# Performance work log

Hardware: AMD Instinct MI355X
Metric: run time of the kernel (lower is better)

Reference implementation:

```python
import jax, jax.numpy as jnp
import numpy as np

N_NODES = 50000
N_EDGES = 600000
IN_DIM = 128
HID = 128
N_CLASSES = 40
N_GRAPHS = 128


def setup_inputs() -> dict:
    key = jax.random.key(0)
    ks = jax.random.split(key, 12)
    x = jax.random.normal(ks[0], (N_NODES, IN_DIM), dtype=jnp.float32)
    edge_index = jax.random.randint(ks[1], (2, N_EDGES), 0, N_NODES, dtype=jnp.int64)
    batch = jnp.sort(jax.random.randint(ks[2], (N_NODES,), 0, N_GRAPHS, dtype=jnp.int64))
    dims = [IN_DIM, HID, HID, N_CLASSES]
    params = {}
    for l in range(3):
        d_in, d_out = dims[l], dims[l + 1]
        s = 1.0 / np.sqrt(d_in)
        params[f"Wl{l}"] = jax.random.uniform(ks[3 + 3 * l], (d_out, d_in), jnp.float32, -s, s)
        params[f"bl{l}"] = jax.random.uniform(ks[4 + 3 * l], (d_out,), jnp.float32, -s, s)
        params[f"Wr{l}"] = jax.random.uniform(ks[5 + 3 * l], (d_out, d_in), jnp.float32, -s, s)
    return {"x": x, "edge_index": edge_index, "batch": batch, **params}


def _sage_layer(h, src, dst, Wl, bl, Wr):
    # message: relu(x_j) (edge_attr is None -> zero), mean-aggregate at dst
    m = jnp.maximum(h[src], 0.0)                       # [E, d]
    agg = jax.ops.segment_sum(m, dst, num_segments=N_NODES)
    cnt = jax.ops.segment_sum(jnp.ones((m.shape[0],), h.dtype), dst, num_segments=N_NODES)
    agg = agg / jnp.maximum(cnt, 1.0)[:, None]
    # lin_l(agg) + lin_r(x)
    return agg @ Wl.T + bl + h @ Wr.T


def reference(x, edge_index, batch, Wl0, bl0, Wr0, Wl1, bl1, Wr1, Wl2, bl2, Wr2):
    src, dst = edge_index[0], edge_index[1]
    Ws = [(Wl0, bl0, Wr0), (Wl1, bl1, Wr1), (Wl2, bl2, Wr2)]
    h = x
    for l, (Wl, bl, Wr) in enumerate(Ws):
        # dropout is identity in eval mode
        h = _sage_layer(h, src, dst, Wl, bl, Wr)
        if l != len(Ws) - 1:
            h = jnp.maximum(h, 0.0)
    # global mean pool over graphs
    gsum = jax.ops.segment_sum(h, batch, num_segments=N_GRAPHS)
    gcnt = jax.ops.segment_sum(jnp.ones((h.shape[0],), h.dtype), batch, num_segments=N_GRAPHS)
    g = gsum / jnp.maximum(gcnt, 1.0)[:, None]
    return h, g
```

## Files before the change

### kernel.cpp

```cpp
#include <hip/hip_runtime.h>
#include <hip/hip_bf16.h>


#define NODES 50000
#define K_DIM 128
#define N_GRAPHS 128

typedef __attribute__((ext_vector_type(8))) short short8;
typedef __attribute__((ext_vector_type(4))) short short4v;
typedef __attribute__((ext_vector_type(4))) float f32x4;

__device__ inline short f2bf(float f) {
    unsigned u = __builtin_bit_cast(unsigned, f);
    u += 0x7FFFu + ((u >> 16) & 1u);
    return (short)(u >> 16);
}
__device__ inline float bf2f(short h) {
    unsigned u = ((unsigned)(unsigned short)h) << 16;
    return __builtin_bit_cast(float, u);
}
__device__ inline float blo(unsigned u) { return __builtin_bit_cast(float, u << 16); }
__device__ inline float bhi(unsigned u) { return __builtin_bit_cast(float, u & 0xFFFF0000u); }
__device__ inline unsigned hilo_pack(float f) {
    short h = f2bf(f);
    short l = f2bf(f - bf2f(h));
    return ((unsigned)(unsigned short)h) | (((unsigned)(unsigned short)l) << 16);
}

__global__ void init_kernel(const float* __restrict__ w0, const float* __restrict__ w1,
                            const float* __restrict__ w2, const float* __restrict__ w3,
                            const float* __restrict__ w4, const float* __restrict__ w5,
                            short* __restrict__ whi, short* __restrict__ wlo,
                            int* __restrict__ deg, const int* __restrict__ batch,
                            int* __restrict__ gstart,
                            const float* __restrict__ x, short* __restrict__ xb, int N) {
    int idx = blockIdx.x * 256 + threadIdx.x;
    if (idx < N * (K_DIM / 4)) {
        float4 v = reinterpret_cast<const float4*>(x)[idx];
        short4v b;
        b[0] = f2bf(fmaxf(v.x, 0.f));
        b[1] = f2bf(fmaxf(v.y, 0.f));
        b[2] = f2bf(fmaxf(v.z, 0.f));
        b[3] = f2bf(fmaxf(v.w, 0.f));
        *reinterpret_cast<short4v*>(&xb[idx * 4]) = b;
    }
    if (idx < N) deg[idx] = 0;
    const int TOT = 4 * 16384 + 96 * 128;
    if (idx < TOT) {
        float v;
        if (idx < 65536) {
            int m = idx >> 14, e = idx & 16383;
            const float* W = (m == 0) ? w0 : (m == 1) ? w1 : (m == 2) ? w2 : w3;
            v = W[e];
        } else {
            int i2 = idx - 65536;
            int row = i2 >> 7, col = i2 & 127;
            if (row < 40)      v = w4[row * 128 + col];
            else if (row < 80) v = w5[(row - 40) * 128 + col];
            else               v = 0.f;
        }
        unsigned p = hilo_pack(v);
        whi[idx] = (short)(p & 0xFFFFu);
        wlo[idx] = (short)(p >> 16);
    }
    if (idx <= N_GRAPHS) {
        int g = idx;
        int lo = 0, hi = N;
        while (lo < hi) {
            int mid = (lo + hi) >> 1;
            if (batch[mid] < g) lo = mid + 1; else hi = mid;
        }
        gstart[g] = lo;
    }
}

__global__ void deg_kernel(const int* __restrict__ dst, int* __restrict__ deg, int E) {
    int e = blockIdx.x * blockDim.x + threadIdx.x;
    if (e < E) atomicAdd(&deg[dst[e]], 1);
}

__global__ void scan_p1(const int* __restrict__ deg, int* __restrict__ bsum, int N) {
    int i = blockIdx.x * 256 + threadIdx.x;
    int v = (i < N) ? deg[i] : 0;
    #pragma unroll
    for (int off = 32; off > 0; off >>= 1) v += __shfl_down(v, off, 64);
    __shared__ int ws[4];
    int lane = threadIdx.x & 63, wv = threadIdx.x >> 6;
    if (lane == 0) ws[wv] = v;
    __syncthreads();
    if (threadIdx.x == 0) bsum[blockIdx.x] = ws[0] + ws[1] + ws[2] + ws[3];
}

__global__ void scan_p23(const int* __restrict__ deg, const int* __restrict__ bsum,
                         int* __restrict__ rowptr, int* __restrict__ fillpos,
                         int N, int NB) {
    const int tid = threadIdx.x, lane = tid & 63, wv = tid >> 6;
    __shared__ int ws[4];
    __shared__ int sboff[256];
    {
        int v = (tid < NB) ? bsum[tid] : 0;
        int incl = v;
        #pragma unroll
        for (int off = 1; off < 64; off <<= 1) {
            int t = __shfl_up(incl, off, 64);
            if (lane >= off) incl += t;
        }
        if (lane == 63) ws[wv] = incl;
        __syncthreads();
        int add = 0;
        for (int k = 0; k < wv; ++k) add += ws[k];
        sboff[tid] = incl + add - v;
        __syncthreads();
    }
    const int boff = sboff[blockIdx.x];
    int i = blockIdx.x * 256 + tid;
    int v = (i < N) ? deg[i] : 0;
    int incl = v;
    #pragma unroll
    for (int off = 1; off < 64; off <<= 1) {
        int t = __shfl_up(incl, off, 64);
        if (lane >= off) incl += t;
    }
    __shared__ int ws2[4];
    if (lane == 63) ws2[wv] = incl;
    __syncthreads();
    int add = 0;
    for (int k = 0; k < wv; ++k) add += ws2[k];
    int excl = boff + incl + add - v;
    if (i < N) { rowptr[i] = excl; fillpos[i] = excl; }
    if (i == N) rowptr[N] = excl;
}

__global__ void fill_kernel(const int* __restrict__ src, const int* __restrict__ dst,
                            int* __restrict__ fillpos, int* __restrict__ csr_src, int E) {
    int e = blockIdx.x * blockDim.x + threadIdx.x;
    if (e < E) {
        int p = atomicAdd(&fillpos[dst[e]], 1);
        csr_src[p] = src[e];
    }
}

__global__ void agg_bf16(const unsigned short* __restrict__ hb,
                         const int* __restrict__ rowptr,
                         const int* __restrict__ csr_src,
                         float* __restrict__ agg, int N) {
    int w = (blockIdx.x * blockDim.x + threadIdx.x) >> 6;
    if (w >= N) return;
    int lane = threadIdx.x & 63;
    int half = lane >> 5, l32 = lane & 31;
    int s = rowptr[w], e = rowptr[w + 1];
    float4 acc = make_float4(0.f, 0.f, 0.f, 0.f);
    int i = s + half;
    for (; i + 6 < e; i += 8) {
        int s0 = csr_src[i], s1 = csr_src[i + 2], s2 = csr_src[i + 4], s3 = csr_src[i + 6];
        uint2 v0 = reinterpret_cast<const uint2*>(hb + (size_t)s0 * K_DIM)[l32];
        uint2 v1 = reinterpret_cast<const uint2*>(hb + (size_t)s1 * K_DIM)[l32];
        uint2 v2 = reinterpret_cast<const uint2*>(hb + (size_t)s2 * K_DIM)[l32];
        uint2 v3 = reinterpret_cast<const uint2*>(hb + (size_t)s3 * K_DIM)[l32];
        acc.x += (blo(v0.x) + blo(v1.x)) + (blo(v2.x) + blo(v3.x));
        acc.y += (bhi(v0.x) + bhi(v1.x)) + (bhi(v2.x) + bhi(v3.x));
        acc.z += (blo(v0.y) + blo(v1.y)) + (blo(v2.y) + blo(v3.y));
        acc.w += (bhi(v0.y) + bhi(v1.y)) + (bhi(v2.y) + bhi(v3.y));
    }
    for (; i < e; i += 2) {
        int s0 = csr_src[i];
        uint2 v0 = reinterpret_cast<const uint2*>(hb + (size_t)s0 * K_DIM)[l32];
        acc.x += blo(v0.x); acc.y += bhi(v0.x);
        acc.z += blo(v0.y); acc.w += bhi(v0.y);
    }
    acc.x += __shfl_xor(acc.x, 32, 64);
    acc.y += __shfl_xor(acc.y, 32, 64);
    acc.z += __shfl_xor(acc.z, 32, 64);
    acc.w += __shfl_xor(acc.w, 32, 64);
    if (half == 0) {
        float inv = 1.0f / fmaxf((float)(e - s), 1.0f);
        acc.x *= inv; acc.y *= inv; acc.z *= inv; acc.w *= inv;
        reinterpret_cast<float4*>(agg + (size_t)w * K_DIM)[l32] = acc;
    }
}

template <int WAVES_M, int WAVES_N, int WM_TILES, int WN_TILES, bool BF16OUT>
__global__ __launch_bounds__(256) void sage_mfma(
        const float* __restrict__ A, const float* __restrict__ H,
        const short* __restrict__ Bhl, const short* __restrict__ Bll,
        const short* __restrict__ Bhr, const short* __restrict__ Blr,
        const float* __restrict__ bl, float* __restrict__ out,
        short* __restrict__ outb, int N) {
    constexpr int BM = WAVES_M * WM_TILES * 16;
    constexpr int LSTR = 40;
    const int tid = threadIdx.x;
    const int lane = tid & 63;
    const int wave = tid >> 6;
    const int wm = wave % WAVES_M;
    const int wn = wave / WAVES_M;
    const int l15 = lane & 15;
    const int quad = lane >> 4;
    const int m0 = blockIdx.x * BM;

    __shared__ __align__(16) short Ahi[BM * LSTR];
    __shared__ __align__(16) short Alo[BM * LSTR];

    f32x4 acc[WM_TILES][WN_TILES];
    #pragma unroll
    for (int i = 0; i < WM_TILES; ++i)
        #pragma unroll
        for (int j = 0; j < WN_TILES; ++j)
            acc[i][j] = (f32x4){0.f, 0.f, 0.f, 0.f};

    #pragma unroll
    for (int ph = 0; ph < 2; ++ph) {
        const float* __restrict__ X = ph ? H : A;
        const short* __restrict__ Bh = ph ? Bhr : Bhl;
        const short* __restrict__ Bv = ph ? Blr : Bll;
        for (int k0 = 0; k0 < K_DIM; k0 += 32) {
            __syncthreads();
            #pragma unroll
            for (int r = 0; r < BM * 8 / 256; ++r) {
                int idx = r * 256 + tid;
                int row = idx >> 3, c4 = idx & 7;
                int m = m0 + row;
                float4 v = make_float4(0.f, 0.f, 0.f, 0.f);
                if (m < N) v = *reinterpret_cast<const float4*>(X + (size_t)m * K_DIM + k0 + c4 * 4);
                unsigned px = hilo_pack(v.x);
                unsigned py = hilo_pack(v.y);
                unsigned pz = hilo_pack(v.z);
                unsigned pw = hilo_pack(v.w);
                short4v h4, l4;
                h4[0] = (short)(px & 0xFFFFu); l4[0] = (short)(px >> 16);
                h4[1] = (short)(py & 0xFFFFu); l4[1] = (short)(py >> 16);
                h4[2] = (short)(pz & 0xFFFFu); l4[2] = (short)(pz >> 16);
                h4[3] = (short)(pw & 0xFFFFu); l4[3] = (short)(pw >> 16);
                *reinterpret_cast<short4v*>(&Ahi[row * LSTR + c4 * 4]) = h4;
                *reinterpret_cast<short4v*>(&Alo[row * LSTR + c4 * 4]) = l4;
            }
            short8 bh[WN_TILES], bo[WN_TILES];
            #pragma unroll
            for (int nt = 0; nt < WN_TILES; ++nt) {
                int n = wn * WN_TILES * 16 + nt * 16 + l15;
                bh[nt] = *reinterpret_cast<const short8*>(Bh + (size_t)n * K_DIM + k0 + quad * 8);
                bo[nt] = *reinterpret_cast<const short8*>(Bv + (size_t)n * K_DIM + k0 + quad * 8);
            }
            __syncthreads();
            #pragma unroll
            for (int mt = 0; mt < WM_TILES; ++mt) {
                int row = wm * WM_TILES * 16 + mt * 16 + l15;
                short8 ah = *reinterpret_cast<const short8*>(&Ahi[row * LSTR + quad * 8]);
                short8 ao = *reinterpret_cast<const short8*>(&Alo[row * LSTR + quad * 8]);
                #pragma unroll
                for (int nt = 0; nt < WN_TILES; ++nt) {
                    acc[mt][nt] = __builtin_amdgcn_mfma_f32_16x16x32_bf16(ah, bh[nt], acc[mt][nt], 0, 0, 0);
                    acc[mt][nt] = __builtin_amdgcn_mfma_f32_16x16x32_bf16(ah, bo[nt], acc[mt][nt], 0, 0, 0);
                    acc[mt][nt] = __builtin_amdgcn_mfma_f32_16x16x32_bf16(ao, bh[nt], acc[mt][nt], 0, 0, 0);
                }
            }
        }
    }

    #pragma unroll
    for (int mt = 0; mt < WM_TILES; ++mt) {
        #pragma unroll
        for (int nt = 0; nt < WN_TILES; ++nt) {
            int col = wn * WN_TILES * 16 + nt * 16 + l15;
            float b = bl[col];
            #pragma unroll
            for (int reg = 0; reg < 4; ++reg) {
                int row = m0 + wm * WM_TILES * 16 + mt * 16 + quad * 4 + reg;
                if (row < N) {
                    float v = fmaxf(acc[mt][nt][reg] + b, 0.f);
                    out[(size_t)row * K_DIM + col] = v;
                    if (BF16OUT) outb[(size_t)row * K_DIM + col] = f2bf(v);
                }
            }
        }
    }
}

__global__ __launch_bounds__(256) void gemm80(
        const float* __restrict__ X, const short* __restrict__ Bh,
        const short* __restrict__ Bv, const float* __restrict__ b2,
        short* __restrict__ ylb, float* __restrict__ yr40, int N) {
    constexpr int BM = 64;
    constexpr int LSTR = 40;
    const int tid = threadIdx.x;
    const int lane = tid & 63;
    const int wave = tid >> 6;
    const int wm = wave & 1;
    const int wn = wave >> 1;
    const int l15 = lane & 15;
    const int quad = lane >> 4;
    const int m0 = blockIdx.x * BM;

    __shared__ __align__(16) short Ahi[BM * LSTR];
    __shared__ __align__(16) short Alo[BM * LSTR];

    f32x4 acc[2][3];
    #pragma unroll
    for (int i = 0; i < 2; ++i)
        #pragma unroll
        for (int j = 0; j < 3; ++j) acc[i][j] = (f32x4){0.f, 0.f, 0.f, 0.f};

    for (int k0 = 0; k0 < K_DIM; k0 += 32) {
        __syncthreads();
        #pragma unroll
        for (int r = 0; r < 2; ++r) {
            int idx = r * 256 + tid;
            int row = idx >> 3, c4 = idx & 7;
            int m = m0 + row;
            float4 v = make_float4(0.f, 0.f, 0.f, 0.f);
            if (m < N) v = *reinterpret_cast<const float4*>(X + (size_t)m * K_DIM + k0 + c4 * 4);
            unsigned px = hilo_pack(v.x);
            unsigned py = hilo_pack(v.y);
            unsigned pz = hilo_pack(v.z);
            unsigned pw = hilo_pack(v.w);
            short4v h4, l4;
            h4[0] = (short)(px & 0xFFFFu); l4[0] = (short)(px >> 16);
            h4[1] = (short)(py & 0xFFFFu); l4[1] = (short)(py >> 16);
            h4[2] = (short)(pz & 0xFFFFu); l4[2] = (short)(pz >> 16);
            h4[3] = (short)(pw & 0xFFFFu); l4[3] = (short)(pw >> 16);
            *reinterpret_cast<short4v*>(&Ahi[row * LSTR + c4 * 4]) = h4;
            *reinterpret_cast<short4v*>(&Alo[row * LSTR + c4 * 4]) = l4;
        }
        __syncthreads();
        short8 bh[3], bo[3];
        #pragma unroll
        for (int nt = 0; nt < 3; ++nt) {
            int n = wn * 48 + nt * 16 + l15;
            bh[nt] = *reinterpret_cast<const short8*>(Bh + (size_t)n * K_DIM + k0 + quad * 8);
            bo[nt] = *reinterpret_cast<const short8*>(Bv + (size_t)n * K_DIM + k0 + quad * 8);
        }
        #pragma unroll
        for (int mt = 0; mt < 2; ++mt) {
            int row = wm * 32 + mt * 16 + l15;
            short8 ah = *reinterpret_cast<const short8*>(&Ahi[row * LSTR + quad * 8]);
            short8 ao = *reinterpret_cast<const short8*>(&Alo[row * LSTR + quad * 8]);
            #pragma unroll
            for (int nt = 0; nt < 3; ++nt) {
                acc[mt][nt] = __builtin_amdgcn_mfma_f32_16x16x32_bf16(ah, bh[nt], acc[mt][nt], 0, 0, 0);
                acc[mt][nt] = __builtin_amdgcn_mfma_f32_16x16x32_bf16(ah, bo[nt], acc[mt][nt], 0, 0, 0);
                acc[mt][nt] = __builtin_amdgcn_mfma_f32_16x16x32_bf16(ao, bh[nt], acc[mt][nt], 0, 0, 0);
            }
        }
    }

    #pragma unroll
    for (int mt = 0; mt < 2; ++mt) {
        #pragma unroll
        for (int nt = 0; nt < 3; ++nt) {
            int col = wn * 48 + nt * 16 + l15;
            #pragma unroll
            for (int reg = 0; reg < 4; ++reg) {
                int row = m0 + wm * 32 + mt * 16 + quad * 4 + reg;
                if (row < N) {
                    float v = acc[mt][nt][reg];
                    if (col < 40) {
                        ylb[(size_t)row * 40 + col] = f2bf(v);
                    } else if (col < 80) {
                        yr40[(size_t)row * 40 + (col - 40)] = v + b2[col - 40];
                    }
                }
            }
        }
    }
}

__global__ void agg40_kernel(const unsigned short* __restrict__ ylb,
                             const float* __restrict__ yr40,
                             const int* __restrict__ rowptr, const int* __restrict__ csr_src,
                             float* __restrict__ out, int N) {
    int w = (blockIdx.x * blockDim.x + threadIdx.x) >> 6;
    if (w >= N) return;
    int lane = threadIdx.x & 63;
    int s = rowptr[w], e = rowptr[w + 1];
    if (lane >= 40) return;
    float acc = 0.f;
    int i = s;
    for (; i + 3 < e; i += 4) {
        int s0 = csr_src[i], s1 = csr_src[i + 1], s2 = csr_src[i + 2], s3 = csr_src[i + 3];
        float v0 = bf2f((short)ylb[(size_t)s0 * 40 + lane]);
        float v1 = bf2f((short)ylb[(size_t)s1 * 40 + lane]);
        float v2 = bf2f((short)ylb[(size_t)s2 * 40 + lane]);
        float v3 = bf2f((short)ylb[(size_t)s3 * 40 + lane]);
        acc += (v0 + v1) + (v2 + v3);
    }
    for (; i < e; ++i) acc += bf2f((short)ylb[(size_t)csr_src[i] * 40 + lane]);
    float inv = 1.0f / fmaxf((float)(e - s), 1.0f);
    out[(size_t)w * 40 + lane] = acc * inv + yr40[(size_t)w * 40 + lane];
}

__global__ __launch_bounds__(320) void pool_kernel(const float* __restrict__ h,
                                                   const int* __restrict__ gstart,
                                                   float* __restrict__ g_out) {
    int g = blockIdx.x;
    int tid = threadIdx.x;
    int c = tid % 40, r = tid / 40;
    int s = gstart[g], e = gstart[g + 1];
    float acc = 0.f;
    for (int n = s + r; n < e; n += 8)
        acc += h[(size_t)n * 40 + c];
    __shared__ float sh[8][40];
    sh[r][c] = acc;
    __syncthreads();
    if (r == 0) {
        float sum = 0.f;
        #pragma unroll
        for (int i = 0; i < 8; ++i) sum += sh[i][c];
        g_out[g * 40 + c] = sum / fmaxf((float)(e - s), 1.0f);
    }
}

extern "C" void kernel_launch(void* const* d_in, const int* in_sizes, int n_in,
                              void* d_out, int out_size, void* d_ws, size_t ws_size,
                              hipStream_t stream) {
    const float* x    = (const float*)d_in[0];
    const int*   ei   = (const int*)d_in[1];
    const int*   batch= (const int*)d_in[2];
    const float* Wl0  = (const float*)d_in[3];
    const float* bl0  = (const float*)d_in[4];
    const float* Wr0  = (const float*)d_in[5];
    const float* Wl1  = (const float*)d_in[6];
    const float* bl1  = (const float*)d_in[7];
    const float* Wr1  = (const float*)d_in[8];
    const float* Wl2  = (const float*)d_in[9];
    const float* bl2  = (const float*)d_in[10];
    const float* Wr2  = (const float*)d_in[11];

    const int N = in_sizes[0] / K_DIM;
    const int E = in_sizes[1] / 2;
    const int* src = ei;
    const int* dst = ei + E;

    float* out = (float*)d_out;
    float* gsum = out + (size_t)N * 40;

    char* w = (char*)d_ws;
    auto alloc = [&](size_t bytes) {
        char* p = w;
        w += (bytes + 255) & ~(size_t)255;
        return p;
    };
    float* bufA  = (float*)alloc((size_t)N * K_DIM * 4);
    float* bufB  = (float*)alloc((size_t)N * K_DIM * 4);
    float* bufC  = (float*)alloc((size_t)N * K_DIM * 4);
    short* ylb   = (short*)alloc((size_t)N * 40 * 2);
    float* yr40  = (float*)alloc((size_t)N * 40 * 4);
    int*   rowptr= (int*)alloc((size_t)(N + 1) * 4);
    int*   deg   = (int*)alloc((size_t)N * 4);
    int*   fillp = (int*)alloc((size_t)N * 4);
    int*   csr   = (int*)alloc((size_t)E * 4);
    int*   bsum  = (int*)alloc(256 * 4);
    int*   gstart= (int*)alloc((size_t)(N_GRAPHS + 1) * 4);
    short* whi   = (short*)alloc(77824 * 2);
    short* wlo   = (short*)alloc(77824 * 2);

    short* xb  = (short*)bufC;
    short* h1b = (short*)bufC + (size_t)N * K_DIM;

    const int NB = (N + 255) / 256;
    const int initGrid = (N * (K_DIM / 4) + 255) / 256;

    init_kernel<<<initGrid, 256, 0, stream>>>(Wl0, Wr0, Wl1, Wr1, Wl2, Wr2,
                                              whi, wlo, deg, batch, gstart, x, xb, N);
    deg_kernel<<<(E + 255) / 256, 256, 0, stream>>>(dst, deg, E);
    scan_p1<<<NB, 256, 0, stream>>>(deg, bsum, N);
    scan_p23<<<NB, 256, 0, stream>>>(deg, bsum, rowptr, fillp, N, NB);
    fill_kernel<<<(E + 255) / 256, 256, 0, stream>>>(src, dst, fillp, csr, E);

    short* hWl0 = whi;          short* lWl0 = wlo;
    short* hWr0 = whi + 16384;  short* lWr0 = wlo + 16384;
    short* hWl1 = whi + 32768;  short* lWl1 = wlo + 32768;
    short* hWr1 = whi + 49152;  short* lWr1 = wlo + 49152;
    short* hW2  = whi + 65536;  short* lW2  = wlo + 65536;

    const int aggGrid  = (N * 64 + 255) / 256;
    const int gemmGrid = (N + 63) / 64;

    agg_bf16<<<aggGrid, 256, 0, stream>>>((const unsigned short*)xb, rowptr, csr, bufA, N);
    sage_mfma<1, 4, 4, 2, true><<<gemmGrid, 256, 0, stream>>>(
        bufA, x, hWl0, lWl0, hWr0, lWr0, bl0, bufB, h1b, N);
    agg_bf16<<<aggGrid, 256, 0, stream>>>((const unsigned short*)h1b, rowptr, csr, bufA, N);
    sage_mfma<1, 4, 4, 2, false><<<gemmGrid, 256, 0, stream>>>(
        bufA, bufB, hWl1, lWl1, hWr1, lWr1, bl1, bufC, nullptr, N);
    gemm80<<<gemmGrid, 256, 0, stream>>>(bufC, hW2, lW2, bl2, ylb, yr40, N);
    agg40_kernel<<<aggGrid, 256, 0, stream>>>((const unsigned short*)ylb, yr40, rowptr, csr, out, N);

    pool_kernel<<<N_GRAPHS, 320, 0, stream>>>(out, gstart, gsum);
}
```

Measured before the change: 337.0 us.

## Store intermediate activations as precomputed bf16 hi/lo split planes

Activations between layers are now written as separate bf16 high and low planes instead of fp32, so the GEMMs load ready-made bf16 tiles rather than splitting fp32 in their staging loop. The aggregation output is stored as a single bf16 plane and multiplied with only the hi/lo weight terms, which drops the low-part activation MFMA for the aggregated operand. The input x is also split in the init kernel. This cuts global memory traffic and conversion ALU work, but the aggregated operand loses precision.

After: 335.9 us (median of 2 runs). About the same (-0.3%).

```diff
diff --git a/kernel.cpp b/kernel.cpp
--- a/kernel.cpp
+++ b/kernel.cpp
@@ -33,16 +33,21 @@
                             short* __restrict__ whi, short* __restrict__ wlo,
                             int* __restrict__ deg, const int* __restrict__ batch,
                             int* __restrict__ gstart,
-                            const float* __restrict__ x, short* __restrict__ xb, int N) {
+                            const float* __restrict__ x, short* __restrict__ xb,
+                            short* __restrict__ xhi, short* __restrict__ xlo, int N) {
     int idx = blockIdx.x * 256 + threadIdx.x;
     if (idx < N * (K_DIM / 4)) {
         float4 v = reinterpret_cast<const float4*>(x)[idx];
-        short4v b;
-        b[0] = f2bf(fmaxf(v.x, 0.f));
-        b[1] = f2bf(fmaxf(v.y, 0.f));
-        b[2] = f2bf(fmaxf(v.z, 0.f));
-        b[3] = f2bf(fmaxf(v.w, 0.f));
-        *reinterpret_cast<short4v*>(&xb[idx * 4]) = b;
+        unsigned px = hilo_pack(v.x), py = hilo_pack(v.y);
+        unsigned pz = hilo_pack(v.z), pw = hilo_pack(v.w);
+        short4v b, hh, ll;
+        b[0] = f2bf(fmaxf(v.x, 0.f)); hh[0] = (short)(px & 0xFFFFu); ll[0] = (short)(px >> 16);
+        b[1] = f2bf(fmaxf(v.y, 0.f)); hh[1] = (short)(py & 0xFFFFu); ll[1] = (short)(py >> 16);
+        b[2] = f2bf(fmaxf(v.z, 0.f)); hh[2] = (short)(pz & 0xFFFFu); ll[2] = (short)(pz >> 16);
+        b[3] = f2bf(fmaxf(v.w, 0.f)); hh[3] = (short)(pw & 0xFFFFu); ll[3] = (short)(pw >> 16);
+        *reinterpret_cast<short4v*>(&xb [idx * 4]) = b;
+        *reinterpret_cast<short4v*>(&xhi[idx * 4]) = hh;
+        *reinterpret_cast<short4v*>(&xlo[idx * 4]) = ll;
     }
     if (idx < N) deg[idx] = 0;
     const int TOT = 4 * 16384 + 96 * 128;
@@ -143,7 +148,7 @@
 __global__ void agg_bf16(const unsigned short* __restrict__ hb,
                          const int* __restrict__ rowptr,
                          const int* __restrict__ csr_src,
-                         float* __restrict__ agg, int N) {
+                         short* __restrict__ aggb, int N) {
     int w = (blockIdx.x * blockDim.x + threadIdx.x) >> 6;
     if (w >= N) return;
     int lane = threadIdx.x & 63;
@@ -174,101 +179,118 @@
     acc.w += __shfl_xor(acc.w, 32, 64);
     if (half == 0) {
         float inv = 1.0f / fmaxf((float)(e - s), 1.0f);
-        acc.x *= inv; acc.y *= inv; acc.z *= inv; acc.w *= inv;
-        reinterpret_cast<float4*>(agg + (size_t)w * K_DIM)[l32] = acc;
-    }
-}
-
-template <int WAVES_M, int WAVES_N, int WM_TILES, int WN_TILES, bool BF16OUT>
+        short4v b;
+        b[0] = f2bf(acc.x * inv);
+        b[1] = f2bf(acc.y * inv);
+        b[2] = f2bf(acc.z * inv);
+        b[3] = f2bf(acc.w * inv);
+        *reinterpret_cast<short4v*>(&aggb[(size_t)w * K_DIM + l32 * 4]) = b;
+    }
+}
+
 __global__ __launch_bounds__(256) void sage_mfma(
-        const float* __restrict__ A, const float* __restrict__ H,
+        const short* __restrict__ Ab_in,
+        const short* __restrict__ Hhi_in, const short* __restrict__ Hlo_in,
         const short* __restrict__ Bhl, const short* __restrict__ Bll,
         const short* __restrict__ Bhr, const short* __restrict__ Blr,
-        const float* __restrict__ bl, float* __restrict__ out,
-        short* __restrict__ outb, int N) {
-    constexpr int BM = WAVES_M * WM_TILES * 16;
+        const float* __restrict__ bl,
+        short* __restrict__ outHi, short* __restrict__ outLo, int N) {
+    constexpr int BM = 64;
     constexpr int LSTR = 40;
     const int tid = threadIdx.x;
     const int lane = tid & 63;
     const int wave = tid >> 6;
-    const int wm = wave % WAVES_M;
-    const int wn = wave / WAVES_M;
     const int l15 = lane & 15;
     const int quad = lane >> 4;
     const int m0 = blockIdx.x * BM;
+    const int srow = tid >> 2, sc8 = tid & 3;
 
     __shared__ __align__(16) short Ahi[BM * LSTR];
     __shared__ __align__(16) short Alo[BM * LSTR];
 
-    f32x4 acc[WM_TILES][WN_TILES];
+    f32x4 acc[4][2];
     #pragma unroll
-    for (int i = 0; i < WM_TILES; ++i)
-        #pragma unroll
-        for (int j = 0; j < WN_TILES; ++j)
-            acc[i][j] = (f32x4){0.f, 0.f, 0.f, 0.f};
+    for (int i = 0; i < 4; ++i)
+        #pragma unroll
+        for (int j = 0; j < 2; ++j) acc[i][j] = (f32x4){0.f, 0.f, 0.f, 0.f};
+
+    const short8 zero8 = (short8){0, 0, 0, 0, 0, 0, 0, 0};
+    const int sm = m0 + srow;
+
+    for (int k0 = 0; k0 < K_DIM; k0 += 32) {
+        __syncthreads();
+        {
+            short8 v = zero8;
+            if (sm < N) v = *reinterpret_cast<const short8*>(Ab_in + (size_t)sm * K_DIM + k0 + sc8 * 8);
+            *reinterpret_cast<short8*>(&Ahi[srow * LSTR + sc8 * 8]) = v;
+        }
+        short8 bh[2], bo[2];
+        #pragma unroll
+        for (int nt = 0; nt < 2; ++nt) {
+            int n = wave * 32 + nt * 16 + l15;
+            bh[nt] = *reinterpret_cast<const short8*>(Bhl + (size_t)n * K_DIM + k0 + quad * 8);
+            bo[nt] = *reinterpret_cast<const short8*>(Bll + (size_t)n * K_DIM + k0 + quad * 8);
+        }
+        __syncthreads();
+        #pragma unroll
+        for (int mt = 0; mt < 4; ++mt) {
+            int row = mt * 16 + l15;
+            short8 ab = *reinterpret_cast<const short8*>(&Ahi[row * LSTR + quad * 8]);
+            #pragma unroll
+            for (int nt = 0; nt < 2; ++nt) {
+                acc[mt][nt] = __builtin_amdgcn_mfma_f32_16x16x32_bf16(ab, bh[nt], acc[mt][nt], 0, 0, 0);
+                acc[mt][nt] = __builtin_amdgcn_mfma_f32_16x16x32_bf16(ab, bo[nt], acc[mt][nt], 0, 0, 0);
+            }
+        }
+    }
+
+    for (int k0 = 0; k0 < K_DIM; k0 += 32) {
+        __syncthreads();
+        {
+            short8 vh = zero8, vl = zero8;
+            if (sm < N) {
+                vh = *reinterpret_cast<const short8*>(Hhi_in + (size_t)sm * K_DIM + k0 + sc8 * 8);
+                vl = *reinterpret_cast<const short8*>(Hlo_in + (size_t)sm * K_DIM + k0 + sc8 * 8);
+            }
+            *reinterpret_cast<short8*>(&Ahi[srow * LSTR + sc8 * 8]) = vh;
+            *reinterpret_cast<short8*>(&Alo[srow * LSTR + sc8 * 8]) = vl;
+        }
+        short8 bh[2], bo[2];
+        #pragma unroll
+        for (int nt = 0; nt < 2; ++nt) {
+            int n = wave * 32 + nt * 16 + l15;
+            bh[nt] = *reinterpret_cast<const short8*>(Bhr + (size_t)n * K_DIM + k0 + quad * 8);
+            bo[nt] = *reinterpret_cast<const short8*>(Blr + (size_t)n * K_DIM + k0 + quad * 8);
+        }
+        __syncthreads();
+        #pragma unroll
+        for (int mt = 0; mt < 4; ++mt) {
+            int row = mt * 16 + l15;
+            short8 ah = *reinterpret_cast<const short8*>(&Ahi[row * LSTR + quad * 8]);
+            short8 ao = *reinterpret_cast<const short8*>(&Alo[row * LSTR + quad * 8]);
+            #pragma unroll
+            for (int nt = 0; nt < 2; ++nt) {
+                acc[mt][nt] = __builtin_amdgcn_mfma_f32_16x16x32_bf16(ah, bh[nt], acc[mt][nt], 0, 0, 0);
+                acc[mt][nt] = __builtin_amdgcn_mfma_f32_16x16x32_bf16(ah, bo[nt], acc[mt][nt], 0, 0, 0);
+                acc[mt][nt] = __builtin_amdgcn_mfma_f32_16x16x32_bf16(ao, bh[nt], acc[mt][nt], 0, 0, 0);
+            }
+        }
+    }
 
     #pragma unroll
-    for (int ph = 0; ph < 2; ++ph) {
-        const float* __restrict__ X = ph ? H : A;
-        const short* __restrict__ Bh = ph ? Bhr : Bhl;
-        const short* __restrict__ Bv = ph ? Blr : Bll;
-        for (int k0 = 0; k0 < K_DIM; k0 += 32) {
-            __syncthreads();
-            #pragma unroll
-            for (int r = 0; r < BM * 8 / 256; ++r) {
-                int idx = r * 256 + tid;
-                int row = idx >> 3, c4 = idx & 7;
-                int m = m0 + row;
-                float4 v = make_float4(0.f, 0.f, 0.f, 0.f);
-                if (m < N) v = *reinterpret_cast<const float4*>(X + (size_t)m * K_DIM + k0 + c4 * 4);
-                unsigned px = hilo_pack(v.x);
-                unsigned py = hilo_pack(v.y);
-                unsigned pz = hilo_pack(v.z);
-                unsigned pw = hilo_pack(v.w);
-                short4v h4, l4;
-                h4[0] = (short)(px & 0xFFFFu); l4[0] = (short)(px >> 16);
-                h4[1] = (short)(py & 0xFFFFu); l4[1] = (short)(py >> 16);
-                h4[2] = (short)(pz & 0xFFFFu); l4[2] = (short)(pz >> 16);
-                h4[3] = (short)(pw & 0xFFFFu); l4[3] = (short)(pw >> 16);
-                *reinterpret_cast<short4v*>(&Ahi[row * LSTR + c4 * 4]) = h4;
-                *reinterpret_cast<short4v*>(&Alo[row * LSTR + c4 * 4]) = l4;
-            }
-            short8 bh[WN_TILES], bo[WN_TILES];
-            #pragma unroll
-            for (int nt = 0; nt < WN_TILES; ++nt) {
-                int n = wn * WN_TILES * 16 + nt * 16 + l15;
-                bh[nt] = *reinterpret_cast<const short8*>(Bh + (size_t)n * K_DIM + k0 + quad * 8);
-                bo[nt] = *reinterpret_cast<const short8*>(Bv + (size_t)n * K_DIM + k0 + quad * 8);
-            }
-            __syncthreads();
-            #pragma unroll
-            for (int mt = 0; mt < WM_TILES; ++mt) {
-                int row = wm * WM_TILES * 16 + mt * 16 + l15;
-                short8 ah = *reinterpret_cast<const short8*>(&Ahi[row * LSTR + quad * 8]);
-                short8 ao = *reinterpret_cast<const short8*>(&Alo[row * LSTR + quad * 8]);
-                #pragma unroll
-                for (int nt = 0; nt < WN_TILES; ++nt) {
-                    acc[mt][nt] = __builtin_amdgcn_mfma_f32_16x16x32_bf16(ah, bh[nt], acc[mt][nt], 0, 0, 0);
-                    acc[mt][nt] = __builtin_amdgcn_mfma_f32_16x16x32_bf16(ah, bo[nt], acc[mt][nt], 0, 0, 0);
-                    acc[mt][nt] = __builtin_amdgcn_mfma_f32_16x16x32_bf16(ao, bh[nt], acc[mt][nt], 0, 0, 0);
-                }
-            }
-        }
-    }
-
-    #pragma unroll
-    for (int mt = 0; mt < WM_TILES; ++mt) {
-        #pragma unroll
-        for (int nt = 0; nt < WN_TILES; ++nt) {
-            int col = wn * WN_TILES * 16 + nt * 16 + l15;
+    for (int mt = 0; mt < 4; ++mt) {
+        #pragma unroll
+        for (int nt = 0; nt < 2; ++nt) {
+            int col = wave * 32 + nt * 16 + l15;
             float b = bl[col];
             #pragma unroll
             for (int reg = 0; reg < 4; ++reg) {
-                int row = m0 + wm * WM_TILES * 16 + mt * 16 + quad * 4 + reg;
+                int row = m0 + mt * 16 + quad * 4 + reg;
                 if (row < N) {
                     float v = fmaxf(acc[mt][nt][reg] + b, 0.f);
-                    out[(size_t)row * K_DIM + col] = v;
-                    if (BF16OUT) outb[(size_t)row * K_DIM + col] = f2bf(v);
+                    unsigned p = hilo_pack(v);
+                    outHi[(size_t)row * K_DIM + col] = (short)(p & 0xFFFFu);
+                    outLo[(size_t)row * K_DIM + col] = (short)(p >> 16);
                 }
             }
         }
@@ -276,8 +298,9 @@
 }
 
 __global__ __launch_bounds__(256) void gemm80(
-        const float* __restrict__ X, const short* __restrict__ Bh,
-        const short* __restrict__ Bv, const float* __restrict__ b2,
+        const short* __restrict__ Xhi, const short* __restrict__ Xlo,
+        const short* __restrict__ Bh, const short* __restrict__ Bv,
+        const float* __restrict__ b2,
         short* __restrict__ ylb, float* __restrict__ yr40, int N) {
     constexpr int BM = 64;
     constexpr int LSTR = 40;
@@ -289,6 +312,7 @@
     const int l15 = lane & 15;
     const int quad = lane >> 4;
     const int m0 = blockIdx.x * BM;
+    const int srow = tid >> 2, sc8 = tid & 3;
 
     __shared__ __align__(16) short Ahi[BM * LSTR];
     __shared__ __align__(16) short Alo[BM * LSTR];
@@ -299,28 +323,20 @@
         #pragma unroll
         for (int j = 0; j < 3; ++j) acc[i][j] = (f32x4){0.f, 0.f, 0.f, 0.f};
 
+    const short8 zero8 = (short8){0, 0, 0, 0, 0, 0, 0, 0};
+    const int sm = m0 + srow;
+
     for (int k0 = 0; k0 < K_DIM; k0 += 32) {
         __syncthreads();
-        #pragma unroll
-        for (int r = 0; r < 2; ++r) {
-            int idx = r * 256 + tid;
-            int row = idx >> 3, c4 = idx & 7;
-            int m = m0 + row;
-            float4 v = make_float4(0.f, 0.f, 0.f, 0.f);
-            if (m < N) v = *reinterpret_cast<const float4*>(X + (size_t)m * K_DIM + k0 + c4 * 4);
-            unsigned px = hilo_pack(v.x);
-            unsigned py = hilo_pack(v.y);
-            unsigned pz = hilo_pack(v.z);
-            unsigned pw = hilo_pack(v.w);
-            short4v h4, l4;
-            h4[0] = (short)(px & 0xFFFFu); l4[0] = (short)(px >> 16);
-            h4[1] = (short)(py & 0xFFFFu); l4[1] = (short)(py >> 16);
-            h4[2] = (short)(pz & 0xFFFFu); l4[2] = (short)(pz >> 16);
-            h4[3] = (short)(pw & 0xFFFFu); l4[3] = (short)(pw >> 16);
-            *reinterpret_cast<short4v*>(&Ahi[row * LSTR + c4 * 4]) = h4;
-            *reinterpret_cast<short4v*>(&Alo[row * LSTR + c4 * 4]) = l4;
-        }
-        __syncthreads();
+        {
+            short8 vh = zero8, vl = zero8;
+            if (sm < N) {
+                vh = *reinterpret_cast<const short8*>(Xhi + (size_t)sm * K_DIM + k0 + sc8 * 8);
+                vl = *reinterpret_cast<const short8*>(Xlo + (size_t)sm * K_DIM + k0 + sc8 * 8);
+            }
+            *reinterpret_cast<short8*>(&Ahi[srow * LSTR + sc8 * 8]) = vh;
+            *reinterpret_cast<short8*>(&Alo[srow * LSTR + sc8 * 8]) = vl;
+        }
         short8 bh[3], bo[3];
         #pragma unroll
         for (int nt = 0; nt < 3; ++nt) {
@@ -328,6 +344,7 @@
             bh[nt] = *reinterpret_cast<const short8*>(Bh + (size_t)n * K_DIM + k0 + quad * 8);
             bo[nt] = *reinterpret_cast<const short8*>(Bv + (size_t)n * K_DIM + k0 + quad * 8);
         }
+        __syncthreads();
         #pragma unroll
         for (int mt = 0; mt < 2; ++mt) {
             int row = wm * 32 + mt * 16 + l15;
@@ -438,9 +455,15 @@
         w += (bytes + 255) & ~(size_t)255;
         return p;
     };
-    float* bufA  = (float*)alloc((size_t)N * K_DIM * 4);
-    float* bufB  = (float*)alloc((size_t)N * K_DIM * 4);
-    float* bufC  = (float*)alloc((size_t)N * K_DIM * 4);
+    const size_t PL = (size_t)N * K_DIM * 2;
+    short* aggb  = (short*)alloc(PL);
+    short* xb    = (short*)alloc(PL);
+    short* xhi   = (short*)alloc(PL);
+    short* xlo   = (short*)alloc(PL);
+    short* h1hi  = (short*)alloc(PL);
+    short* h1lo  = (short*)alloc(PL);
+    short* h2hi  = (short*)alloc(PL);
+    short* h2lo  = (short*)alloc(PL);
     short* ylb   = (short*)alloc((size_t)N * 40 * 2);
     float* yr40  = (float*)alloc((size_t)N * 40 * 4);
     int*   rowptr= (int*)alloc((size_t)(N + 1) * 4);
@@ -452,14 +475,12 @@
     short* whi   = (short*)alloc(77824 * 2);
     short* wlo   = (short*)alloc(77824 * 2);
 
-    short* xb  = (short*)bufC;
-    short* h1b = (short*)bufC + (size_t)N * K_DIM;
-
     const int NB = (N + 255) / 256;
     const int initGrid = (N * (K_DIM / 4) + 255) / 256;
 
     init_kernel<<<initGrid, 256, 0, stream>>>(Wl0, Wr0, Wl1, Wr1, Wl2, Wr2,
-                                              whi, wlo, deg, batch, gstart, x, xb, N);
+                                              whi, wlo, deg, batch, gstart,
+                                              x, xb, xhi, xlo, N);
     deg_kernel<<<(E + 255) / 256, 256, 0, stream>>>(dst, deg, E);
     scan_p1<<<NB, 256, 0, stream>>>(deg, bsum, N);
     scan_p23<<<NB, 256, 0, stream>>>(deg, bsum, rowptr, fillp, N, NB);
@@ -474,13 +495,13 @@
     const int aggGrid  = (N * 64 + 255) / 256;
     const int gemmGrid = (N + 63) / 64;
 
-    agg_bf16<<<aggGrid, 256, 0, stream>>>((const unsigned short*)xb, rowptr, csr, bufA, N);
-    sage_mfma<1, 4, 4, 2, true><<<gemmGrid, 256, 0, stream>>>(
-        bufA, x, hWl0, lWl0, hWr0, lWr0, bl0, bufB, h1b, N);
-    agg_bf16<<<aggGrid, 256, 0, stream>>>((const unsigned short*)h1b, rowptr, csr, bufA, N);
-    sage_mfma<1, 4, 4, 2, false><<<gemmGrid, 256, 0, stream>>>(
-        bufA, bufB, hWl1, lWl1, hWr1, lWr1, bl1, bufC, nullptr, N);
-    gemm80<<<gemmGrid, 256, 0, stream>>>(bufC, hW2, lW2, bl2, ylb, yr40, N);
+    agg_bf16<<<aggGrid, 256, 0, stream>>>((const unsigned short*)xb, rowptr, csr, aggb, N);
+    sage_mfma<<<gemmGrid, 256, 0, stream>>>(
+        aggb, xhi, xlo, hWl0, lWl0, hWr0, lWr0, bl0, h1hi, h1lo, N);
+    agg_bf16<<<aggGrid, 256, 0, stream>>>((const unsigned short*)h1hi, rowptr, csr, aggb, N);
+    sage_mfma<<<gemmGrid, 256, 0, stream>>>(
+        aggb, h1hi, h1lo, hWl1, lWl1, hWr1, lWr1, bl1, h2hi, h2lo, N);
+    gemm80<<<gemmGrid, 256, 0, stream>>>(h2hi, h2lo, hW2, lW2, bl2, ylb, yr40, N);
     agg40_kernel<<<aggGrid, 256, 0, stream>>>((const unsigned short*)ylb, yr40, rowptr, csr, out, N);
 
     pool_kernel<<<N_GRAPHS, 320, 0, stream>>>(out, gstart, gsum);
```
